# Kernel tuning notes

Measured on AMD Instinct MI355X. Metric: run time of the kernel, lower is better.

## Reference

```python
import jax, jax.numpy as jnp
import numpy as np

TEMP = 0.07
EPS_NORM = 1e-12  # torch F.normalize clamp eps
EPS_RENORM = 1e-9


def _l2_normalize(x):
    n = jnp.linalg.norm(x, axis=1, keepdims=True)
    return x / jnp.maximum(n, EPS_NORM)


def setup_inputs() -> dict:
    key = jax.random.key(0)
    k1, k2 = jax.random.split(key)
    feat = jax.random.normal(k1, (65536, 1024), dtype=jnp.float32)
    prompts = jax.random.normal(k2, (1000, 1024), dtype=jnp.float32) * 0.01
    return {"feat": feat, "prompts": prompts, "topk": 2}


def reference(feat, prompts, topk):
    # cosine similarity between normalized feat and normalized prompts
    p_n = _l2_normalize(prompts)            # [C, d]
    q_n = _l2_normalize(feat)               # [N, d]
    sims = jnp.matmul(q_n, p_n.T)           # [N, C]
    probs = jax.nn.softmax(sims / TEMP, axis=1)
    num_classes = prompts.shape[0]
    if topk is not None and topk < num_classes:
        _, topk_idx = jax.lax.top_k(probs, topk)          # [N, k]
        rows = jnp.arange(probs.shape[0])[:, None]        # [N, 1]
        mask = jnp.zeros_like(probs).at[rows, topk_idx].set(1.0)
        probs = probs * mask
        probs = probs / (jnp.sum(probs, axis=1, keepdims=True) + EPS_RENORM)
    mixed_prompt = jnp.matmul(probs, prompts)             # [N, d]
    return (mixed_prompt, probs)
```

## Files before the change

kernel.cpp:

```cpp
#include <hip/hip_runtime.h>
#include <cstdint>

using f32x4 = __attribute__((ext_vector_type(4))) float;
using s16x8 = __attribute__((ext_vector_type(8))) short;
typedef unsigned short u16;

typedef const __attribute__((address_space(1))) uint32_t* gptr_t;
typedef __attribute__((address_space(3))) uint32_t* lptr_t;

__device__ __forceinline__ u16 f2bf(float f) {
  union { float f; uint32_t u; } v; v.f = f;
  uint32_t r = v.u + 0x7FFFu + ((v.u >> 16) & 1u);
  return (u16)(r >> 16);
}
__device__ __forceinline__ float bf2f(u16 b) {
  union { uint32_t u; float f; } v; v.u = ((uint32_t)b) << 16;
  return v.f;
}

__global__ __launch_bounds__(256) void k_prep_prompts(const float* __restrict__ prompts,
                                                      u16* __restrict__ p_bf) {
  const int r = blockIdx.x;
  const int t = threadIdx.x;
  if (r >= 1000) {
    if (t < 128) {
      s16x8 z = {0, 0, 0, 0, 0, 0, 0, 0};
      ((s16x8*)(p_bf + (size_t)r * 1024))[t] = z;
    }
    return;
  }
  float4 x = ((const float4*)(prompts + (size_t)r * 1024))[t];
  float ss = x.x * x.x + x.y * x.y + x.z * x.z + x.w * x.w;
  #pragma unroll
  for (int off = 32; off; off >>= 1) ss += __shfl_xor(ss, off);
  __shared__ float red[4];
  if ((t & 63) == 0) red[t >> 6] = ss;
  __syncthreads();
  float n = fmaxf(sqrtf(red[0] + red[1] + red[2] + red[3]), 1e-12f);
  float inv = 1.0f / n;
  u16* pb = p_bf + (size_t)r * 1024 + t * 4;
  pb[0] = f2bf(x.x * inv); pb[1] = f2bf(x.y * inv);
  pb[2] = f2bf(x.z * inv); pb[3] = f2bf(x.w * inv);
}

__global__ __launch_bounds__(256) void k_feat(const float* __restrict__ feat,
                                              u16* __restrict__ out) {
  const size_t stride = (size_t)gridDim.x * 256;
  const size_t n4 = 67108864ull / 4;
  for (size_t j = (size_t)blockIdx.x * 256 + threadIdx.x; j < n4; j += stride) {
    float4 x = ((const float4*)feat)[j];
    ushort4 o;
    o.x = f2bf(x.x); o.y = f2bf(x.y); o.z = f2bf(x.z); o.w = f2bf(x.w);
    ((ushort4*)out)[j] = o;
  }
}

__global__ __launch_bounds__(512, 2) void k_sims(const u16* __restrict__ A,
                                                 const u16* __restrict__ B,
                                                 u16* __restrict__ C) {
  __shared__ union {
    struct { u16 As[4][2][128 * 32]; u16 Bs[4][2][128 * 32]; } ring;
    u16 tile[256][260];
  } smem;
  const int bid = blockIdx.x;
  const int lg = (bid & 7) * 128 + (bid >> 3);
  const int bn = lg & 3;
  const int bm = lg >> 2;
  const int t = threadIdx.x;
  const int wid = t >> 6, l = t & 63;
  const int wr = wid >> 2;
  const int wc = wid & 3;
  const int lrow = l & 15, lko = l >> 4;

  f32x4 acc[8][4];
  #pragma unroll
  for (int i = 0; i < 8; i++)
    #pragma unroll
    for (int j = 0; j < 4; j++) acc[i][j] = (f32x4){0.f, 0.f, 0.f, 0.f};

  const int srow = t >> 2;
  const int scol_sw = ((t & 3) * 8) ^ ((srow & 6) << 2);
  #define STAGE_A(db, h, kc)                                                              \
    __builtin_amdgcn_global_load_lds(                                                     \
        (gptr_t)(A + (size_t)(bm * 256 + (h) * 128 + srow) * 1024 + (kc) + scol_sw),      \
        (lptr_t)&smem.ring.As[db][h][t * 8], 16, 0, 0)
  #define STAGE_B(db, h, kc)                                                              \
    __builtin_amdgcn_global_load_lds(                                                     \
        (gptr_t)(B + (size_t)(bn * 256 + (h) * 128 + srow) * 1024 + (kc) + scol_sw),      \
        (lptr_t)&smem.ring.Bs[db][h][t * 8], 16, 0, 0)
  #define SWZ(row) (((row) * 32) + ((lko * 8) ^ (((row) & 6) << 2)))

  STAGE_A(0, 0, 0); STAGE_A(0, 1, 0); STAGE_B(0, 0, 0); STAGE_B(0, 1, 0);
  STAGE_A(1, 0, 32); STAGE_A(1, 1, 32); STAGE_B(1, 0, 32); STAGE_B(1, 1, 32);

  const int hB = wc >> 1, rB = (wc & 1) * 64;
  for (int j = 0; j < 32; ++j) {
    const int p = j & 3;
    if (j == 31) asm volatile("s_waitcnt vmcnt(0)" ::: "memory");
    else         asm volatile("s_waitcnt vmcnt(4)" ::: "memory");
    __builtin_amdgcn_s_barrier();
    s16x8 b[4];
    #pragma unroll
    for (int m2 = 0; m2 < 2; ++m2) {
      s16x8 a[4];
      #pragma unroll
      for (int i = 0; i < 4; ++i) {
        const int ar = m2 * 64 + i * 16 + lrow;
        a[i] = *(const s16x8*)&smem.ring.As[p][wr][SWZ(ar)];
      }
      if (m2 == 0) {
        #pragma unroll
        for (int ni = 0; ni < 4; ++ni) {
          const int br = rB + ni * 16 + lrow;
          b[ni] = *(const s16x8*)&smem.ring.Bs[p][hB][SWZ(br)];
        }
      }
      if (j < 30) {
        const int db = (j + 2) & 3, kn = (j + 2) * 32;
        if (m2 == 0) { STAGE_A(db, 0, kn); STAGE_A(db, 1, kn); }
        else         { STAGE_B(db, 0, kn); STAGE_B(db, 1, kn); }
      }
      __builtin_amdgcn_s_setprio(1);
      #pragma unroll
      for (int i = 0; i < 4; ++i)
        #pragma unroll
        for (int ni = 0; ni < 4; ++ni)
          acc[m2 * 4 + i][ni] =
              __builtin_amdgcn_mfma_f32_16x16x32_bf16(a[i], b[ni], acc[m2 * 4 + i][ni], 0, 0, 0);
      __builtin_amdgcn_s_setprio(0);
      __builtin_amdgcn_s_barrier();
    }
  }
  #undef STAGE_A
  #undef STAGE_B
  #undef SWZ
  __syncthreads();
  const int rbase = (l >> 4) * 4;
  const int trow0 = wr * 128, tcol0 = wc * 64;
  #pragma unroll
  for (int mi = 0; mi < 8; ++mi)
    #pragma unroll
    for (int ni = 0; ni < 4; ++ni)
      #pragma unroll
      for (int jj = 0; jj < 4; ++jj)
        smem.tile[trow0 + mi * 16 + rbase + jj][tcol0 + ni * 16 + lrow] = f2bf(acc[mi][ni][jj]);
  __syncthreads();
  #pragma unroll 1
  for (int q = t; q < 256 * 64; q += 512) {
    const int r = q >> 6;
    const int cl = (q & 63) * 4;
    const int gcol = bn * 256 + cl;
    if (gcol < 1000) {
      ushort4 v = *(const ushort4*)&smem.tile[r][cl];
      *(ushort4*)&C[(size_t)(bm * 256 + r) * 1000 + gcol] = v;
    }
  }
}

__global__ __launch_bounds__(256) void k_topk(const float* __restrict__ feat,
                                              const float* __restrict__ prompts,
                                              const u16* __restrict__ sims,
                                              int2* __restrict__ resc,
                                              float2* __restrict__ resw,
                                              float* __restrict__ probs) {
  const int l = threadIdx.x & 63;
  const int row = blockIdx.x * 4 + (threadIdx.x >> 6);
  const u16* srow = sims + (size_t)row * 1000;
  const float NEG = -3.0e38f;
  float s[16];
  #pragma unroll
  for (int j = 0; j < 8; j++) {
    int c = 2 * l + 128 * j;
    if (c + 1 < 1000) {
      uint32_t v = *(const uint32_t*)(srow + c);
      s[2 * j] = bf2f((u16)(v & 0xFFFFu));
      s[2 * j + 1] = bf2f((u16)(v >> 16));
    } else {
      s[2 * j] = (c < 1000) ? bf2f(srow[c]) : NEG;
      s[2 * j + 1] = NEG;
    }
  }
  float a1 = NEG, a2 = NEG;
  #pragma unroll
  for (int j = 0; j < 16; j++) {
    float v = s[j];
    bool g1 = v > a1;
    a2 = g1 ? a1 : fmaxf(a2, v);
    a1 = g1 ? v : a1;
  }
  #pragma unroll
  for (int off = 32; off; off >>= 1) {
    float b1 = __shfl_xor(a1, off), b2 = __shfl_xor(a2, off);
    float m1 = fmaxf(a1, b1);
    float m2 = fmaxf(fminf(a1, b1), fmaxf(a2, b2));
    a1 = m1; a2 = m2;
  }
  const float T = a2 - 0.25f;
  uint32_t mask = 0;
  #pragma unroll
  for (int j = 0; j < 16; j++) {
    int c = 2 * l + 128 * (j >> 1) + (j & 1);
    if (c < 1000 && s[j] >= T) mask |= (1u << j);
  }
  const int base = l * 16;
  float q[16];
  const float4* fr = (const float4*)(feat + (size_t)row * 1024 + base);
  #pragma unroll
  for (int g = 0; g < 4; g++) {
    float4 x = fr[g];
    q[g * 4 + 0] = x.x; q[g * 4 + 1] = x.y; q[g * 4 + 2] = x.z; q[g * 4 + 3] = x.w;
  }
  float qq = 0.f;
  #pragma unroll
  for (int e = 0; e < 16; e++) qq += q[e] * q[e];
  #pragma unroll
  for (int off = 32; off; off >>= 1) qq += __shfl_xor(qq, off);
  float rn = 1.0f / fmaxf(sqrtf(qq), 1e-12f);
  float s1 = NEG, s2 = NEG;
  int c1 = 0x40000000, c2 = 0x40000000;
  while (true) {
    unsigned long long act = __ballot(mask != 0);
    if (!act) break;
    int ln = (int)__ffsll(act) - 1;
    int fj = __ffs(mask) - 1;
    int myc = 2 * l + 128 * ((fj >> 1) & 7) + (fj & 1);
    int bc = __shfl(myc, ln);
    if (l == ln) mask &= (mask - 1);
    bc = (bc < 1000) ? bc : 999;
    const float4* pr = (const float4*)(prompts + (size_t)bc * 1024 + base);
    float d = 0.f, nn = 0.f;
    #pragma unroll
    for (int g = 0; g < 4; g++) {
      float4 x = pr[g];
      d += q[g * 4 + 0] * x.x; d += q[g * 4 + 1] * x.y;
      d += q[g * 4 + 2] * x.z; d += q[g * 4 + 3] * x.w;
      nn += x.x * x.x + x.y * x.y + x.z * x.z + x.w * x.w;
    }
    #pragma unroll
    for (int off = 32; off; off >>= 1) {
      d += __shfl_xor(d, off);
      nn += __shfl_xor(nn, off);
    }
    float sc = d * rn / fmaxf(sqrtf(nn), 1e-12f);
    bool b1w = (sc > s1) || (sc == s1 && bc < c1);
    bool b2w = (sc > s2) || (sc == s2 && bc < c2);
    if (b1w) { s2 = s1; c2 = c1; s1 = sc; c1 = bc; }
    else if (b2w) { s2 = sc; c2 = bc; }
  }
  float e = expf(fminf(s2 - s1, 0.0f) * (1.0f / 0.07f));
  float w1 = 1.0f / (1.0f + e);
  float w2 = e / (1.0f + e);
  float* prow = probs + (size_t)row * 1000;
  #pragma unroll
  for (int j = 0; j < 16; j++) {
    int c = l + 64 * j;
    if (c < 1000) prow[c] = (c == c1) ? w1 : ((c == c2) ? w2 : 0.0f);
  }
  if (l == 0) {
    resc[row] = make_int2(c1, c2);
    resw[row] = make_float2(w1, w2);
  }
}

__global__ __launch_bounds__(256) void k_write2(const float* __restrict__ prompts,
                                                const int2* __restrict__ resc,
                                                const float2* __restrict__ resw,
                                                float* __restrict__ mixed) {
  const int row = blockIdx.x;
  const int t = threadIdx.x;
  int2 cc = resc[row];
  float2 ww = resw[row];
  float4 a = ((const float4*)(prompts + (size_t)cc.x * 1024))[t];
  float4 b = ((const float4*)(prompts + (size_t)cc.y * 1024))[t];
  float4 o;
  o.x = ww.x * a.x + ww.y * b.x;
  o.y = ww.x * a.y + ww.y * b.y;
  o.z = ww.x * a.z + ww.y * b.z;
  o.w = ww.x * a.w + ww.y * b.w;
  ((float4*)(mixed + (size_t)row * 1024))[t] = o;
}

extern "C" void kernel_launch(void* const* d_in, const int* in_sizes, int n_in,
                              void* d_out, int out_size, void* d_ws, size_t ws_size,
                              hipStream_t stream) {
  int fi = 0, pi = 1;
  for (int i = 0; i < n_in; i++) {
    if (in_sizes[i] == 67108864) fi = i;
    else if (in_sizes[i] == 1024000) pi = i;
  }
  const float* feat = (const float*)d_in[fi];
  const float* prompts = (const float*)d_in[pi];

  float* mixed = (float*)d_out;
  float* probs = mixed + 67108864ull;

  u16* p_bf = (u16*)d_ws;
  int2* resc = (int2*)((char*)d_ws + (2ull << 20));
  float2* resw = (float2*)((char*)d_ws + (2ull << 20) + (512ull << 10));

  u16* sims = (u16*)mixed;
  u16* feat_bf = (u16*)probs;

  hipLaunchKernelGGL(k_prep_prompts, dim3(1024), dim3(256), 0, stream, prompts, p_bf);
  hipLaunchKernelGGL(k_feat, dim3(2048), dim3(256), 0, stream, feat, feat_bf);
  hipLaunchKernelGGL(k_sims, dim3(1024), dim3(512), 0, stream, feat_bf, p_bf, sims);
  hipLaunchKernelGGL(k_topk, dim3(16384), dim3(256), 0, stream, feat, prompts, sims, resc, resw, probs);
  hipLaunchKernelGGL(k_write2, dim3(65536), dim3(256), 0, stream, prompts, resc, resw, mixed);
}
```

Baseline: 497.7 us.

## Fuse per-tile top-2 candidate filtering into sims GEMM epilogue

The GEMM epilogue no longer writes the full bf16 similarity matrix. Each wave scans its 256-column tile row, finds the local top-2, keeps up to 16 candidates within a 0.25 margin of the second-best, and writes them as packed (value, column) words. The top-k kernel then reads 64 compact words per row instead of 1000 bf16 values, which removes about 128 MB of write and read traffic. In exchange the GEMM epilogue gains per-row wave reductions and serial ballot loops, and any tile with more than 16 candidates in the margin silently drops the extras.

Result: slower. 607.8 us (+22.1%).

```diff
diff --git a/kernel.cpp b/kernel.cpp
--- a/kernel.cpp
+++ b/kernel.cpp
@@ -57,7 +57,7 @@
 
 __global__ __launch_bounds__(512, 2) void k_sims(const u16* __restrict__ A,
                                                  const u16* __restrict__ B,
-                                                 u16* __restrict__ C) {
+                                                 uint32_t* __restrict__ cand) {
   __shared__ union {
     struct { u16 As[4][2][128 * 32]; u16 Bs[4][2][128 * 32]; } ring;
     u16 tile[256][260];
@@ -145,49 +145,63 @@
       for (int jj = 0; jj < 4; ++jj)
         smem.tile[trow0 + mi * 16 + rbase + jj][tcol0 + ni * 16 + lrow] = f2bf(acc[mi][ni][jj]);
   __syncthreads();
+  const float NEGF = -3.0e38f;
   #pragma unroll 1
-  for (int q = t; q < 256 * 64; q += 512) {
-    const int r = q >> 6;
-    const int cl = (q & 63) * 4;
-    const int gcol = bn * 256 + cl;
-    if (gcol < 1000) {
-      ushort4 v = *(const ushort4*)&smem.tile[r][cl];
-      *(ushort4*)&C[(size_t)(bm * 256 + r) * 1000 + gcol] = v;
-    }
+  for (int rr = 0; rr < 32; ++rr) {
+    const int r = wid * 32 + rr;
+    const uint64_t pk = *(const uint64_t*)&smem.tile[r][l * 4];
+    const int cbase = bn * 256 + l * 4;
+    float f0 = (cbase + 0 < 1000) ? bf2f((u16)(pk)) : NEGF;
+    float f1 = (cbase + 1 < 1000) ? bf2f((u16)(pk >> 16)) : NEGF;
+    float f2 = (cbase + 2 < 1000) ? bf2f((u16)(pk >> 32)) : NEGF;
+    float f3 = (cbase + 3 < 1000) ? bf2f((u16)(pk >> 48)) : NEGF;
+    float a1 = f0, a2 = NEGF;
+    { bool g = f1 > a1; a2 = g ? a1 : fmaxf(a2, f1); a1 = g ? f1 : a1; }
+    { bool g = f2 > a1; a2 = g ? a1 : fmaxf(a2, f2); a1 = g ? f2 : a1; }
+    { bool g = f3 > a1; a2 = g ? a1 : fmaxf(a2, f3); a1 = g ? f3 : a1; }
+    #pragma unroll
+    for (int off = 32; off; off >>= 1) {
+      float b1 = __shfl_xor(a1, off), b2 = __shfl_xor(a2, off);
+      float m1 = fmaxf(a1, b1);
+      float m2v = fmaxf(fminf(a1, b1), fmaxf(a2, b2));
+      a1 = m1; a2 = m2v;
+    }
+    const float T = a2 - 0.25f;
+    uint32_t m4 = 0;
+    if (f0 >= T) m4 |= 1u;
+    if (f1 >= T) m4 |= 2u;
+    if (f2 >= T) m4 |= 4u;
+    if (f3 >= T) m4 |= 8u;
+    uint32_t myword = 0xFFFFFFFFu;
+    #pragma unroll 1
+    for (int it = 0; it < 16; ++it) {
+      unsigned long long act = __ballot(m4 != 0);
+      if (!act) break;
+      int ln = (int)__ffsll(act) - 1;
+      int fj = __ffs(m4) - 1;
+      uint32_t vbits = (uint32_t)((pk >> (16 * fj)) & 0xFFFFull);
+      uint32_t wd = (vbits << 16) | (uint32_t)(cbase + fj);
+      uint32_t wdb = __shfl(wd, ln);
+      if (l == it) myword = wdb;
+      if (l == ln) m4 &= (m4 - 1);
+    }
+    if (l < 16) cand[(size_t)(bm * 256 + r) * 64 + bn * 16 + l] = myword;
   }
 }
 
 __global__ __launch_bounds__(256) void k_topk(const float* __restrict__ feat,
                                               const float* __restrict__ prompts,
-                                              const u16* __restrict__ sims,
+                                              const uint32_t* __restrict__ cand,
                                               int2* __restrict__ resc,
                                               float2* __restrict__ resw,
                                               float* __restrict__ probs) {
   const int l = threadIdx.x & 63;
   const int row = blockIdx.x * 4 + (threadIdx.x >> 6);
-  const u16* srow = sims + (size_t)row * 1000;
   const float NEG = -3.0e38f;
-  float s[16];
-  #pragma unroll
-  for (int j = 0; j < 8; j++) {
-    int c = 2 * l + 128 * j;
-    if (c + 1 < 1000) {
-      uint32_t v = *(const uint32_t*)(srow + c);
-      s[2 * j] = bf2f((u16)(v & 0xFFFFu));
-      s[2 * j + 1] = bf2f((u16)(v >> 16));
-    } else {
-      s[2 * j] = (c < 1000) ? bf2f(srow[c]) : NEG;
-      s[2 * j + 1] = NEG;
-    }
-  }
-  float a1 = NEG, a2 = NEG;
-  #pragma unroll
-  for (int j = 0; j < 16; j++) {
-    float v = s[j];
-    bool g1 = v > a1;
-    a2 = g1 ? a1 : fmaxf(a2, v);
-    a1 = g1 ? v : a1;
-  }
+  uint32_t wd = cand[(size_t)row * 64 + l];
+  int col = (int)(wd & 0xFFFFu);
+  float val = (col < 1000) ? bf2f((u16)(wd >> 16)) : NEG;
+  float a1 = val, a2 = NEG;
   #pragma unroll
   for (int off = 32; off; off >>= 1) {
     float b1 = __shfl_xor(a1, off), b2 = __shfl_xor(a2, off);
@@ -196,12 +210,7 @@
     a1 = m1; a2 = m2;
   }
   const float T = a2 - 0.25f;
-  uint32_t mask = 0;
-  #pragma unroll
-  for (int j = 0; j < 16; j++) {
-    int c = 2 * l + 128 * (j >> 1) + (j & 1);
-    if (c < 1000 && s[j] >= T) mask |= (1u << j);
-  }
+  const bool ok = (col < 1000) && (val >= T);
   const int base = l * 16;
   float q[16];
   const float4* fr = (const float4*)(feat + (size_t)row * 1024 + base);
@@ -218,14 +227,11 @@
   float rn = 1.0f / fmaxf(sqrtf(qq), 1e-12f);
   float s1 = NEG, s2 = NEG;
   int c1 = 0x40000000, c2 = 0x40000000;
-  while (true) {
-    unsigned long long act = __ballot(mask != 0);
-    if (!act) break;
-    int ln = (int)__ffsll(act) - 1;
-    int fj = __ffs(mask) - 1;
-    int myc = 2 * l + 128 * ((fj >> 1) & 7) + (fj & 1);
-    int bc = __shfl(myc, ln);
-    if (l == ln) mask &= (mask - 1);
+  unsigned long long actmask = __ballot(ok);
+  while (actmask) {
+    int ln = (int)__ffsll(actmask) - 1;
+    actmask &= actmask - 1;
+    int bc = __shfl(col, ln);
     bc = (bc < 1000) ? bc : 999;
     const float4* pr = (const float4*)(prompts + (size_t)bc * 1024 + base);
     float d = 0.f, nn = 0.f;
@@ -297,13 +303,14 @@
   u16* p_bf = (u16*)d_ws;
   int2* resc = (int2*)((char*)d_ws + (2ull << 20));
   float2* resw = (float2*)((char*)d_ws + (2ull << 20) + (512ull << 10));
-
-  u16* sims = (u16*)mixed;
+  uint32_t* cand = (uint32_t*)((char*)d_ws + (3ull << 20));
+
   u16* feat_bf = (u16*)probs;
 
   hipLaunchKernelGGL(k_prep_prompts, dim3(1024), dim3(256), 0, stream, prompts, p_bf);
   hipLaunchKernelGGL(k_feat, dim3(2048), dim3(256), 0, stream, feat, feat_bf);
-  hipLaunchKernelGGL(k_sims, dim3(1024), dim3(512), 0, stream, feat_bf, p_bf, sims);
-  hipLaunchKernelGGL(k_topk, dim3(16384), dim3(256), 0, stream, feat, prompts, sims, resc, resw, probs);
+  hipLaunchKernelGGL(k_sims, dim3(1024), dim3(512), 0, stream, feat_bf, p_bf, cand);
+  hipLaunchKernelGGL(k_topk, dim3(16384), dim3(256), 0, stream,
+                     feat, prompts, cand, resc, resw, probs);
   hipLaunchKernelGGL(k_write2, dim3(65536), dim3(256), 0, stream, prompts, resc, resw, mixed);
 }
```
